# Performance work log

Hardware: AMD Instinct MI355X
Metric: run time of the kernel (lower is better)

## Reference

```python
import jax, jax.numpy as jnp
import numpy as np
import math

B = 16          # graphs per batch
N = 2048        # nodes per graph
F_IN = 64       # input node features
E_PER = 32768   # edges per graph
E = B * E_PER
H = 128         # hidden width (fixed by module)
C = 10          # output classes
K = math.ceil(0.8 * N)  # TopKPooling keep count per graph = 1639


def setup_inputs() -> dict:
    key = jax.random.key(0)
    ks = jax.random.split(key, 24)
    x = jax.random.normal(ks[0], (B * N, F_IN), jnp.float32)
    # intra-graph random edges (source->target), global node ids
    gid = jnp.repeat(jnp.arange(B, dtype=jnp.int32), E_PER)
    src = gid * N + jax.random.randint(ks[1], (E,), 0, N, dtype=jnp.int32)
    dst = gid * N + jax.random.randint(ks[2], (E,), 0, N, dtype=jnp.int32)

    def lin_w(k, o, i):
        return jax.random.normal(k, (o, i), jnp.float32) / jnp.sqrt(i)

    inp = dict(x=x, src=src, dst=dst)
    # GraphConv: lin_rel (with bias) on aggregated neighbors + lin_root (no bias)
    inp.update(W1_rel=lin_w(ks[3], H, F_IN), b1=jnp.zeros((H,), jnp.float32), W1_root=lin_w(ks[4], H, F_IN))
    inp.update(W2_rel=lin_w(ks[5], H, H), b2=jnp.zeros((H,), jnp.float32), W2_root=lin_w(ks[6], H, H))
    inp.update(W3_rel=lin_w(ks[7], H, H), b3=jnp.zeros((H,), jnp.float32), W3_root=lin_w(ks[8], H, H))
    inp.update(pool_w=jax.random.normal(ks[9], (H,), jnp.float32) / jnp.sqrt(H))
    inp.update(Wl1=lin_w(ks[10], 128, 256), bl1=jnp.zeros((128,), jnp.float32))
    inp.update(Wl2=lin_w(ks[11], 64, 128), bl2=jnp.zeros((64,), jnp.float32))
    inp.update(Wl3=lin_w(ks[12], C, 64), bl3=jnp.zeros((C,), jnp.float32))
    return inp


def _graph_conv(x, src, dst, W_rel, b, W_root, n_nodes, emask=None):
    # out_i = W_rel @ (sum_{j->i} x_j) + b + W_root @ x_i
    msg = x[src]
    if emask is not None:
        msg = msg * emask[:, None]
    agg = jax.ops.segment_sum(msg, dst, num_segments=n_nodes)
    return agg @ W_rel.T + b + x @ W_root.T


def _global_pools(x, n_per_graph):
    xb = x.reshape(B, n_per_graph, -1)
    return jnp.concatenate([xb.max(axis=1), xb.mean(axis=1)], axis=1)  # [B, 2F]


def reference(x, src, dst, W1_rel, b1, W1_root, W2_rel, b2, W2_root,
              W3_rel, b3, W3_root, pool_w, Wl1, bl1, Wl2, bl2, Wl3, bl3):
    n0 = B * N
    h = jax.nn.relu(_graph_conv(x, src, dst, W1_rel, b1, W1_root, n0))
    x1 = _global_pools(h, N)

    h = jax.nn.relu(_graph_conv(h, src, dst, W2_rel, b2, W2_root, n0))

    # TopKPooling(ratio=0.8): score = tanh(x@w/||w||); keep top-k per graph;
    # kept features scaled by score; edges with a dropped endpoint removed.
    score = jnp.tanh((h @ pool_w) / jnp.linalg.norm(pool_w))  # [B*N]
    top_s, top_i = jax.lax.top_k(score.reshape(B, N), K)      # [B,K]
    perm = (top_i + jnp.arange(B)[:, None] * N).reshape(-1)   # global old ids [B*K]
    h = h[perm] * top_s.reshape(-1)[:, None]                  # [B*K, H]

    n1 = B * K
    new_id = jnp.full((n0,), -1, jnp.int32).at[perm].set(jnp.arange(n1, dtype=jnp.int32))
    ns, nd = new_id[src], new_id[dst]
    keep = ((ns >= 0) & (nd >= 0)).astype(h.dtype)
    ns = jnp.where(ns >= 0, ns, 0)
    nd = jnp.where(nd >= 0, nd, 0)

    x2 = _global_pools(h, K)
    h = jax.nn.relu(_graph_conv(h, ns, nd, W3_rel, b3, W3_root, n1, emask=keep))
    x3 = _global_pools(h, K)

    z = x1 + x2 + x3
    z = jax.nn.relu(z @ Wl1.T + bl1)
    z = jax.nn.relu(z @ Wl2.T + bl2)
    return jax.nn.log_softmax(z @ Wl3.T + bl3, axis=-1)  # [B, C]
```

## Files before the change

kernel.cpp:

```cpp
#include <hip/hip_runtime.h>
#include <hip/hip_bf16.h>
#include <math.h>

#define NB 32768
#define NN 2048
#define BG 16
#define KK 1639
#define KKP 1664
#define N1 (BG*KK)
#define N1P (BG*KKP)
#define EE 524288
#define HH 128
#define FIN 64

using half8 = __attribute__((ext_vector_type(8))) _Float16;
using half4 = __attribute__((ext_vector_type(4))) _Float16;
using f32x4 = __attribute__((ext_vector_type(4))) float;

__device__ __forceinline__ void acc4(f32x4& a, const float4& v) {
  a[0] += v.x; a[1] += v.y; a[2] += v.z; a[3] += v.w;
}

__global__ void deg_kernel(const int* __restrict__ dst, int* deg, int n) {
  int e = blockIdx.x * blockDim.x + threadIdx.x;
  if (e < n) atomicAdd(&deg[dst[e]], 1);
}

__global__ void exscan_kernel(const int* __restrict__ deg, int* rs, int* cursor, int n) {
  __shared__ int wsum[16];
  __shared__ int carry;
  int t = threadIdx.x;
  int lane = t & 63, wid = t >> 6;
  if (t == 0) carry = 0;
  __syncthreads();
  int ntiles = (n + 4095) >> 12;
  for (int tile = 0; tile < ntiles; ++tile) {
    int idx = (tile << 12) + t * 4;
    int4 v4 = *(const int4*)(deg + idx);
    int v0 = (idx + 0 < n) ? v4.x : 0;
    int v1 = (idx + 1 < n) ? v4.y : 0;
    int v2 = (idx + 2 < n) ? v4.z : 0;
    int v3 = (idx + 3 < n) ? v4.w : 0;
    int s = v0 + v1 + v2 + v3;
    int pre = s;
#pragma unroll
    for (int off = 1; off < 64; off <<= 1) {
      int u = __shfl_up(pre, off, 64);
      if (lane >= off) pre += u;
    }
    if (lane == 63) wsum[wid] = pre;
    __syncthreads();
    int wbase = 0;
#pragma unroll
    for (int ww = 0; ww < 16; ++ww)
      if (ww < wid) wbase += wsum[ww];
    int ex = carry + wbase + (pre - s);
    int4 e4 = make_int4(ex, ex + v0, ex + v0 + v1, ex + v0 + v1 + v2);
    if (idx + 3 < n) {
      *(int4*)(rs + idx) = e4;
      *(int4*)(cursor + idx) = e4;
    } else {
      if (idx + 0 < n) { rs[idx + 0] = e4.x; cursor[idx + 0] = e4.x; }
      if (idx + 1 < n) { rs[idx + 1] = e4.y; cursor[idx + 1] = e4.y; }
      if (idx + 2 < n) { rs[idx + 2] = e4.z; cursor[idx + 2] = e4.z; }
    }
    int tot = 0;
    if (t == 1023) tot = ex + s;
    __syncthreads();
    if (t == 1023) carry = tot;
    __syncthreads();
  }
  if (t == 0) rs[n] = carry;
}

__global__ void scatter_kernel(const int* __restrict__ src, const int* __restrict__ dst,
                               int* cursor, int* csr, int n) {
  int e = blockIdx.x * blockDim.x + threadIdx.x;
  if (e < n) {
    int d = dst[e];
    int p = atomicAdd(&cursor[d], 1);
    csr[p] = src[e];
  }
}

__global__ void remap_kernel(const int* __restrict__ csr1, const int* __restrict__ new_id,
                             int* __restrict__ csr3, int n) {
  int e = blockIdx.x * blockDim.x + threadIdx.x;
  if (e < n) csr3[e] = new_id[csr1[e]];
}

template <int KD1, int KD2, int POOL, int SCORE, int REMAP>
__global__ __launch_bounds__(512, 4) void conv_mfma(
    const float* __restrict__ feat, const float* __restrict__ xr,
    const int* __restrict__ rs, const int* __restrict__ csr,
    const int* __restrict__ rows3, const int* __restrict__ rowe3,
    const _Float16* __restrict__ Wh, const _Float16* __restrict__ Wl,
    const float* __restrict__ bias, float* __restrict__ out, int M, int nwg,
    float* __restrict__ pmax, float* __restrict__ psum,
    const float* __restrict__ pw, float* __restrict__ score) {
  constexpr int KTOT = KD1 + KD2;
  constexpr int NSTEP = KTOT / 32;
  __shared__ _Float16 ah_lds[64 * KTOT];
  __shared__ _Float16 al_lds[64 * KTOT];
  __shared__ float sdot[64][8];
  __shared__ float swsq[8];

  int tid = threadIdx.x;
  int lane = tid & 63, wid = tid >> 6;
  int bq = nwg >> 3, br = nwg & 7, bx = blockIdx.x & 7, bi = blockIdx.x >> 3;
  int swz = (bx < br ? bx * (bq + 1) : br * (bq + 1) + (bx - br) * bq) + bi;
  int row0 = swz * 64;
  int ch0 = wid * 16;
  int col = lane & 15;
  int kseg = (lane >> 4) * 8;

  {
    constexpr int CH = KD1 / 4;
    constexpr int EPW = 64 / CH;
    int sub = lane / CH;
    int ch = lane % CH;
    const float4* feat4 = (const float4*)feat;
#pragma unroll
    for (int rr = 0; rr < 8; ++rr) {
      int gr = wid * 8 + rr;
      int grow = row0 + gr;
      int e0, e1;
      if (REMAP) {
        e0 = rows3[grow];
        e1 = rowe3[grow];
      } else {
        if (grow >= M) grow = M - 1;
        e0 = rs[grow];
        e1 = rs[grow + 1];
      }
      f32x4 a0 = {0.f, 0.f, 0.f, 0.f}, a1 = a0, a2 = a0, a3 = a0;
      int e = e0 + sub;
      for (; e + 7 * EPW < e1; e += 8 * EPW) {
        int c[8];
#pragma unroll
        for (int u = 0; u < 8; ++u) c[u] = csr[e + u * EPW];
        float4 v[8];
#pragma unroll
        for (int u = 0; u < 8; ++u) {
          int ci = (REMAP && c[u] < 0) ? 0 : c[u];
          v[u] = feat4[(size_t)ci * CH + ch];
        }
        if (REMAP) {
#pragma unroll
          for (int u = 0; u < 8; ++u)
            if (c[u] < 0) v[u] = make_float4(0.f, 0.f, 0.f, 0.f);
        }
        acc4(a0, v[0]); acc4(a1, v[1]); acc4(a2, v[2]); acc4(a3, v[3]);
        acc4(a0, v[4]); acc4(a1, v[5]); acc4(a2, v[6]); acc4(a3, v[7]);
      }
      for (; e + 3 * EPW < e1; e += 4 * EPW) {
        int c[4];
#pragma unroll
        for (int u = 0; u < 4; ++u) c[u] = csr[e + u * EPW];
        float4 v[4];
#pragma unroll
        for (int u = 0; u < 4; ++u) {
          int ci = (REMAP && c[u] < 0) ? 0 : c[u];
          v[u] = feat4[(size_t)ci * CH + ch];
        }
        if (REMAP) {
#pragma unroll
          for (int u = 0; u < 4; ++u)
            if (c[u] < 0) v[u] = make_float4(0.f, 0.f, 0.f, 0.f);
        }
        acc4(a0, v[0]); acc4(a1, v[1]); acc4(a2, v[2]); acc4(a3, v[3]);
      }
      for (; e < e1; e += EPW) {
        int c = csr[e];
        if (REMAP && c < 0) continue;
        float4 v = feat4[(size_t)c * CH + ch];
        acc4(a0, v);
      }
      f32x4 s = (a0 + a1) + (a2 + a3);
      if (EPW == 4) {
#pragma unroll
        for (int j = 0; j < 4; ++j) s[j] += __shfl_xor(s[j], 16, 64);
      }
#pragma unroll
      for (int j = 0; j < 4; ++j) s[j] += __shfl_xor(s[j], 32, 64);
      if (sub == 0) {
        half4 hi, lo;
#pragma unroll
        for (int j = 0; j < 4; ++j) {
          _Float16 h = (_Float16)s[j];
          hi[j] = h;
          lo[j] = (_Float16)(s[j] - (float)h);
        }
        int byte = ((gr * KTOT + ch * 4) * 2) ^ ((gr & 7) << 4);
        *(half4*)((char*)ah_lds + byte) = hi;
        *(half4*)((char*)al_lds + byte) = lo;
      }
    }
  }

  for (int idx = tid; idx < 64 * KD2 / 8; idx += 512) {
    int row = idx / (KD2 / 8);
    int kc = (idx % (KD2 / 8)) * 8;
    int grow = row0 + row;
    if (grow >= M) grow = M - 1;
    const float* sp = xr + (size_t)grow * KD2 + kc;
    float4 a0 = *(const float4*)sp;
    float4 a1 = *(const float4*)(sp + 4);
    float av[8] = {a0.x, a0.y, a0.z, a0.w, a1.x, a1.y, a1.z, a1.w};
    half8 vh, vl;
#pragma unroll
    for (int j = 0; j < 8; ++j) {
      _Float16 h = (_Float16)av[j];
      vh[j] = h;
      vl[j] = (_Float16)(av[j] - (float)h);
    }
    int byte = ((row * KTOT + KD1 + kc) * 2) ^ ((row & 7) << 4);
    *(half8*)((char*)ah_lds + byte) = vh;
    *(half8*)((char*)al_lds + byte) = vl;
  }

  size_t wbase = (size_t)(ch0 + col) * KTOT + kseg;
  half8 whc = *(const half8*)(Wh + wbase);
  half8 wlc = *(const half8*)(Wl + wbase);
  __syncthreads();

  f32x4 acc[4];
#pragma unroll
  for (int rf = 0; rf < 4; ++rf) acc[rf] = (f32x4){0.f, 0.f, 0.f, 0.f};
  int r = lane & 15;
#pragma unroll
  for (int s = 0; s < NSTEP; ++s) {
    half8 whn, wln;
    if (s + 1 < NSTEP) {
      whn = *(const half8*)(Wh + wbase + (s + 1) * 32);
      wln = *(const half8*)(Wl + wbase + (s + 1) * 32);
    }
#pragma unroll
    for (int rf = 0; rf < 4; ++rf) {
      int row = rf * 16 + r;
      int byte = ((row * KTOT + s * 32 + kseg) * 2) ^ ((row & 7) << 4);
      half8 a_h = *(const half8*)((const char*)ah_lds + byte);
      half8 a_l = *(const half8*)((const char*)al_lds + byte);
      acc[rf] = __builtin_amdgcn_mfma_f32_16x16x32_f16(a_l, whc, acc[rf], 0, 0, 0);
      acc[rf] = __builtin_amdgcn_mfma_f32_16x16x32_f16(a_h, wlc, acc[rf], 0, 0, 0);
      acc[rf] = __builtin_amdgcn_mfma_f32_16x16x32_f16(a_h, whc, acc[rf], 0, 0, 0);
    }
    if (s + 1 < NSTEP) { whc = whn; wlc = wln; }
  }

  float bv = bias[ch0 + col];
  float cmax = -3.402823466e38f, csum = 0.f;
  float wcol = SCORE ? pw[ch0 + col] : 0.f;
  float pd[4][4];
  int g = 0, rowbase = 0;
  if (POOL == 2) { g = row0 / KKP; rowbase = row0 - g * KKP; }
#pragma unroll
  for (int rf = 0; rf < 4; ++rf) {
    int orow0 = row0 + rf * 16 + (lane >> 4) * 4;
#pragma unroll
    for (int rr = 0; rr < 4; ++rr) {
      int orow = orow0 + rr;
      float v = fmaxf(acc[rf][rr] + bv, 0.f);
      if (orow < M) out[(size_t)orow * HH + ch0 + col] = v;
      if (POOL == 1) { cmax = fmaxf(cmax, v); csum += v; }
      if (POOL == 2) {
        int local = rowbase + rf * 16 + (lane >> 4) * 4 + rr;
        if (local < KK) { cmax = fmaxf(cmax, v); csum += v; }
      }
      if (SCORE) pd[rf][rr] = v * wcol;
    }
  }
  if (POOL) {
    cmax = fmaxf(cmax, __shfl_xor(cmax, 16, 64)); csum += __shfl_xor(csum, 16, 64);
    cmax = fmaxf(cmax, __shfl_xor(cmax, 32, 64)); csum += __shfl_xor(csum, 32, 64);
    if ((lane >> 4) == 0) {
      if (POOL == 1) {
        int gg = row0 >> 11, sb = (row0 & 2047) >> 6;
        pmax[(gg * 32 + sb) * HH + ch0 + col] = cmax;
        psum[(gg * 32 + sb) * HH + ch0 + col] = csum;
      } else {
        int sb = rowbase >> 6;
        pmax[(g * 26 + sb) * HH + ch0 + col] = cmax;
        psum[(g * 26 + sb) * HH + ch0 + col] = csum;
      }
    }
  }
  if (SCORE) {
#pragma unroll
    for (int rf = 0; rf < 4; ++rf)
#pragma unroll
      for (int rr = 0; rr < 4; ++rr) {
        float d = pd[rf][rr];
        d += __shfl_xor(d, 1, 64); d += __shfl_xor(d, 2, 64);
        d += __shfl_xor(d, 4, 64); d += __shfl_xor(d, 8, 64);
        if (col == 0) sdot[rf * 16 + (lane >> 4) * 4 + rr][wid] = d;
      }
    float wsq = wcol * wcol;
    wsq += __shfl_xor(wsq, 1, 64); wsq += __shfl_xor(wsq, 2, 64);
    wsq += __shfl_xor(wsq, 4, 64); wsq += __shfl_xor(wsq, 8, 64);
    if (lane == 0) swsq[wid] = wsq;
    __syncthreads();
    if (tid < 64) {
      float d = 0.f, q = 0.f;
#pragma unroll
      for (int wv = 0; wv < 8; ++wv) { d += sdot[tid][wv]; q += swsq[wv]; }
      score[row0 + tid] = tanhf(d * rsqrtf(q));
    }
  }
}

__global__ void prep_kernel(const float* __restrict__ W1_rel, const float* __restrict__ W1_root,
                            const float* __restrict__ W2_rel, const float* __restrict__ W2_root,
                            const float* __restrict__ W3_rel, const float* __restrict__ W3_root,
                            _Float16* wh1, _Float16* wl1, _Float16* wh2, _Float16* wl2,
                            _Float16* wh3, _Float16* wl3,
                            int* __restrict__ deg1, int* __restrict__ new_id,
                            int* __restrict__ rows3, int* __restrict__ rowe3) {
  int idx = blockIdx.x * blockDim.x + threadIdx.x;
  if (idx < NB + 4096) deg1[idx] = 0;
  if (idx < NB) new_id[idx] = -1;
  if (idx < N1P) { rows3[idx] = 0; rowe3[idx] = 0; }
  float v;
  _Float16* ph;
  _Float16* pl;
  int j;
  if (idx < 128 * 128) {
    j = idx;
    int o = j >> 7, k = j & 127;
    v = (k < 64) ? W1_rel[o * 64 + k] : W1_root[o * 64 + (k - 64)];
    ph = wh1; pl = wl1;
  } else if (idx < 128 * 128 + 128 * 256) {
    j = idx - 128 * 128;
    int o = j >> 8, k = j & 255;
    v = (k < 128) ? W2_rel[o * 128 + k] : W2_root[o * 128 + (k - 128)];
    ph = wh2; pl = wl2;
  } else if (idx < 128 * 128 + 2 * 128 * 256) {
    j = idx - 128 * 128 - 128 * 256;
    int o = j >> 8, k = j & 255;
    v = (k < 128) ? W3_rel[o * 128 + k] : W3_root[o * 128 + (k - 128)];
    ph = wh3; pl = wl3;
  } else {
    return;
  }
  _Float16 h = (_Float16)v;
  ph[j] = h;
  pl[j] = (_Float16)(v - (float)h);
}

__global__ void topk_kernel(const float* __restrict__ score, int* perm) {
  __shared__ unsigned long long keys[NN];
  __shared__ int hist[256];
  __shared__ unsigned long long sP;
  __shared__ int srem;
  __shared__ int scnt;
  int b = blockIdx.x, t = threadIdx.x;
  for (int i = t; i < NN; i += 256) {
    float s = score[b * NN + i];
    unsigned u = __float_as_uint(s);
    u = (u & 0x80000000u) ? ~u : (u | 0x80000000u);
    keys[i] = ((unsigned long long)u << 32) | (unsigned)(NN - 1 - i);
  }
  if (t == 0) { sP = 0ULL; srem = KK; scnt = 0; }
  __syncthreads();
  for (int pass = 0; pass < 8; ++pass) {
    int shift = 56 - 8 * pass;
    for (int i = t; i < 256; i += 256) hist[i] = 0;
    __syncthreads();
    unsigned long long P = sP;
    unsigned long long hm = (pass == 0) ? 0ULL : (~0ULL) << (shift + 8);
    for (int i = t; i < NN; i += 256) {
      unsigned long long k = keys[i];
      if (((k ^ P) & hm) == 0) atomicAdd(&hist[(int)((k >> shift) & 255)], 1);
    }
    __syncthreads();
    if (t < 64) {
      int l = t;
      int c[4], part = 0;
#pragma unroll
      for (int q = 0; q < 4; ++q) { c[q] = hist[255 - (l * 4 + q)]; part += c[q]; }
      int pre = part;
#pragma unroll
      for (int off = 1; off < 64; off <<= 1) {
        int u2 = __shfl_up(pre, off, 64);
        if (l >= off) pre += u2;
      }
      int excl = pre - part;
      int rem = srem;
      if (excl < rem && rem <= excl + part) {
        int run = excl;
#pragma unroll
        for (int q = 0; q < 4; ++q) {
          if (run + c[q] >= rem) {
            srem = rem - run;
            sP = sP | ((unsigned long long)(255 - (l * 4 + q)) << shift);
            break;
          }
          run += c[q];
        }
      }
    }
    __syncthreads();
  }
  unsigned long long T = sP;
  for (int i = t; i < NN; i += 256) {
    if (keys[i] >= T) {
      int pos = atomicAdd(&scnt, 1);
      perm[b * KK + pos] = b * NN + (NN - 1 - (int)(keys[i] & 0xffffffffULL));
    }
  }
}

__global__ void h3_kernel(const float4* __restrict__ h2, const int* __restrict__ perm,
                          const float* __restrict__ score, const int* __restrict__ rs1,
                          float4* __restrict__ h3, int* __restrict__ new_id,
                          int* __restrict__ rows3, int* __restrict__ rowe3) {
  int idx = blockIdx.x * blockDim.x + threadIdx.x;
  if (idx < N1 * 32) {
    int g = idx >> 5, c = idx & 31;
    int b = g / KK, j = g - b * KK;
    int p = perm[g];
    int pj = b * KKP + j;
    if (c == 0) {
      new_id[p] = pj;
      rows3[pj] = rs1[p];
      rowe3[pj] = rs1[p + 1];
    }
    float s = score[p];
    float4 v = h2[(size_t)p * 32 + c];
    v.x *= s; v.y *= s; v.z *= s; v.w *= s;
    h3[(size_t)pj * 32 + c] = v;
  }
}

__global__ void pool2_kernel(const float* __restrict__ h, float* pmax, float* psum) {
  int b = blockIdx.x / 26, s = blockIdx.x % 26;
  int f = threadIdx.x;
  int r0 = s * 64, r1 = min(KK, r0 + 64);
  float m = -3.402823466e38f, sum = 0.f;
  for (int r = r0; r < r1; ++r) {
    float v = h[(size_t)(b * KKP + r) * HH + f];
    m = fmaxf(m, v);
    sum += v;
  }
  pmax[(b * 26 + s) * HH + f] = m;
  psum[(b * 26 + s) * HH + f] = sum;
}

__global__ void mlp_kernel(const float* __restrict__ pm1, const float* __restrict__ ps1,
                           const float* __restrict__ pm2, const float* __restrict__ ps2,
                           const float* __restrict__ pm3, const float* __restrict__ ps3,
                           const float* __restrict__ Wl1, const float* __restrict__ bl1,
                           const float* __restrict__ Wl2, const float* __restrict__ bl2,
                           const float* __restrict__ Wl3, const float* __restrict__ bl3,
                           float* out) {
  __shared__ float z[256], a1[128], a2[64], a3[10], red[2];
  int b = blockIdx.x, t = threadIdx.x;
  float m1 = -3.402823466e38f, m2 = m1, m3 = m1;
  float s1 = 0.f, s2 = 0.f, s3 = 0.f;
  for (int s = 0; s < 32; ++s) {
    int o = (b * 32 + s) * 128 + t;
    m1 = fmaxf(m1, pm1[o]); s1 += ps1[o];
  }
  for (int s = 0; s < 26; ++s) {
    int o = (b * 26 + s) * 128 + t;
    m2 = fmaxf(m2, pm2[o]); s2 += ps2[o];
    m3 = fmaxf(m3, pm3[o]); s3 += ps3[o];
  }
  z[t] = m1 + m2 + m3;
  z[128 + t] = s1 * (1.f / NN) + (s2 + s3) * (1.f / KK);
  __syncthreads();
  {
    float acc = bl1[t];
    for (int q = 0; q < 256; ++q) acc = fmaf(Wl1[t * 256 + q], z[q], acc);
    a1[t] = fmaxf(acc, 0.f);
  }
  __syncthreads();
  if (t < 64) {
    float acc = bl2[t];
    for (int q = 0; q < 128; ++q) acc = fmaf(Wl2[t * 128 + q], a1[q], acc);
    a2[t] = fmaxf(acc, 0.f);
  }
  __syncthreads();
  if (t < 10) {
    float acc = bl3[t];
    for (int q = 0; q < 64; ++q) acc = fmaf(Wl3[t * 64 + q], a2[q], acc);
    a3[t] = acc;
  }
  __syncthreads();
  if (t == 0) {
    float m = a3[0];
    for (int i = 1; i < 10; ++i) m = fmaxf(m, a3[i]);
    float s = 0.f;
    for (int i = 0; i < 10; ++i) s += expf(a3[i] - m);
    red[0] = m;
    red[1] = logf(s);
  }
  __syncthreads();
  if (t < 10) out[b * 10 + t] = a3[t] - red[0] - red[1];
}

extern "C" void kernel_launch(void* const* d_in, const int* in_sizes, int n_in,
                              void* d_out, int out_size, void* d_ws, size_t ws_size,
                              hipStream_t stream) {
  const float* x       = (const float*)d_in[0];
  const int*   src     = (const int*)d_in[1];
  const int*   dst     = (const int*)d_in[2];
  const float* W1_rel  = (const float*)d_in[3];
  const float* b1      = (const float*)d_in[4];
  const float* W1_root = (const float*)d_in[5];
  const float* W2_rel  = (const float*)d_in[6];
  const float* b2      = (const float*)d_in[7];
  const float* W2_root = (const float*)d_in[8];
  const float* W3_rel  = (const float*)d_in[9];
  const float* b3      = (const float*)d_in[10];
  const float* W3_root = (const float*)d_in[11];
  const float* pool_w  = (const float*)d_in[12];
  const float* Wl1     = (const float*)d_in[13];
  const float* bl1     = (const float*)d_in[14];
  const float* Wl2     = (const float*)d_in[15];
  const float* bl2     = (const float*)d_in[16];
  const float* Wl3     = (const float*)d_in[17];
  const float* bl3     = (const float*)d_in[18];
  float* out = (float*)d_out;

  char* w = (char*)d_ws;
  size_t off = 0;
  auto alloc = [&](size_t bytes) -> char* {
    off = (off + 255) & ~(size_t)255;
    char* p = w + off;
    off += bytes;
    return p;
  };
  int* deg1     = (int*)alloc((NB + 4096) * 4);
  int* rs1      = (int*)alloc((NB + 1) * 4);
  int* cursor1  = (int*)alloc(NB * 4);
  int* csr1     = (int*)alloc((size_t)EE * 4);
  int* csr3     = (int*)alloc((size_t)EE * 4);
  int* new_id   = (int*)alloc(NB * 4);
  int* perm     = (int*)alloc(N1 * 4);
  int* rows3    = (int*)alloc(N1P * 4);
  int* rowe3    = (int*)alloc(N1P * 4);
  _Float16* wh1 = (_Float16*)alloc(128 * 128 * 2);
  _Float16* wl1 = (_Float16*)alloc(128 * 128 * 2);
  _Float16* wh2 = (_Float16*)alloc(128 * 256 * 2);
  _Float16* wl2 = (_Float16*)alloc(128 * 256 * 2);
  _Float16* wh3 = (_Float16*)alloc(128 * 256 * 2);
  _Float16* wl3 = (_Float16*)alloc(128 * 256 * 2);
  float* bufA   = (float*)alloc((size_t)NB * HH * 4);
  float* bufB   = (float*)alloc((size_t)NB * HH * 4);
  float* score  = (float*)alloc(NB * 4);
  float* pm1    = (float*)alloc(BG * 32 * HH * 4);
  float* ps1    = (float*)alloc(BG * 32 * HH * 4);
  float* pm2    = (float*)alloc(BG * 26 * HH * 4);
  float* ps2    = (float*)alloc(BG * 26 * HH * 4);
  float* pm3    = (float*)alloc(BG * 26 * HH * 4);
  float* ps3    = (float*)alloc(BG * 26 * HH * 4);
  if (off > ws_size) return;

  const int TB = 256;
  const int egrid = (EE + TB - 1) / TB;

  prep_kernel<<<(128 * 128 + 2 * 128 * 256 + TB - 1) / TB, TB, 0, stream>>>(
      W1_rel, W1_root, W2_rel, W2_root, W3_rel, W3_root, wh1, wl1, wh2, wl2, wh3, wl3,
      deg1, new_id, rows3, rowe3);

  deg_kernel<<<egrid, TB, 0, stream>>>(dst, deg1, EE);
  exscan_kernel<<<1, 1024, 0, stream>>>(deg1, rs1, cursor1, NB);
  scatter_kernel<<<egrid, TB, 0, stream>>>(src, dst, cursor1, csr1, EE);

  conv_mfma<64, 64, 1, 0, 0><<<NB / 64, 512, 0, stream>>>(
      x, x, rs1, csr1, nullptr, nullptr, wh1, wl1, b1, bufA, NB, NB / 64, pm1, ps1,
      nullptr, nullptr);

  conv_mfma<128, 128, 0, 1, 0><<<NB / 64, 512, 0, stream>>>(
      bufA, bufA, rs1, csr1, nullptr, nullptr, wh2, wl2, b2, bufB, NB, NB / 64,
      nullptr, nullptr, pool_w, score);

  topk_kernel<<<BG, 256, 0, stream>>>(score, perm);
  h3_kernel<<<(N1 * 32 + TB - 1) / TB, TB, 0, stream>>>((const float4*)bufB, perm, score,
                                                        rs1, (float4*)bufA, new_id,
                                                        rows3, rowe3);
  remap_kernel<<<egrid, TB, 0, stream>>>(csr1, new_id, csr3, EE);
  pool2_kernel<<<BG * 26, 128, 0, stream>>>(bufA, pm2, ps2);

  conv_mfma<128, 128, 2, 0, 2><<<N1P / 64, 512, 0, stream>>>(
      bufA, bufA, nullptr, csr3, rows3, rowe3, wh3, wl3, b3, bufB, N1P, N1P / 64, pm3, ps3,
      nullptr, nullptr);

  mlp_kernel<<<BG, 128, 0, stream>>>(pm1, ps1, pm2, ps2, pm3, ps3,
                                     Wl1, bl1, Wl2, bl2, Wl3, bl3, out);
}
```

Baseline: 220.5 us.

## Gather neighbor features from fp16 copies in graph conv aggregation

Adds fp16 shadow copies of the input features, the layer-1 output and the pooled layer-3 input. The conv kernels now gather neighbor rows from these half-precision buffers, eight halves per lane, and accumulate in fp32. This halves the bytes moved by the edge gather, which is the dominant memory cost. The price is extra fp16 writes in the producer kernels and a larger prep grid. Rounding the gathered features to fp16 loses precision compared with the former hi/lo fp32 path.

```diff
diff --git a/kernel.cpp b/kernel.cpp
--- a/kernel.cpp
+++ b/kernel.cpp
@@ -16,10 +16,6 @@
 using half8 = __attribute__((ext_vector_type(8))) _Float16;
 using half4 = __attribute__((ext_vector_type(4))) _Float16;
 using f32x4 = __attribute__((ext_vector_type(4))) float;
-
-__device__ __forceinline__ void acc4(f32x4& a, const float4& v) {
-  a[0] += v.x; a[1] += v.y; a[2] += v.z; a[3] += v.w;
-}
 
 __global__ void deg_kernel(const int* __restrict__ dst, int* deg, int n) {
   int e = blockIdx.x * blockDim.x + threadIdx.x;
@@ -89,13 +85,14 @@
   if (e < n) csr3[e] = new_id[csr1[e]];
 }
 
-template <int KD1, int KD2, int POOL, int SCORE, int REMAP>
+template <int KD1, int KD2, int POOL, int SCORE, int REMAP, int OUT16>
 __global__ __launch_bounds__(512, 4) void conv_mfma(
-    const float* __restrict__ feat, const float* __restrict__ xr,
+    const _Float16* __restrict__ feat, const float* __restrict__ xr,
     const int* __restrict__ rs, const int* __restrict__ csr,
     const int* __restrict__ rows3, const int* __restrict__ rowe3,
     const _Float16* __restrict__ Wh, const _Float16* __restrict__ Wl,
-    const float* __restrict__ bias, float* __restrict__ out, int M, int nwg,
+    const float* __restrict__ bias, float* __restrict__ out,
+    _Float16* __restrict__ out16, int M, int nwg,
     float* __restrict__ pmax, float* __restrict__ psum,
     const float* __restrict__ pw, float* __restrict__ score) {
   constexpr int KTOT = KD1 + KD2;
@@ -115,11 +112,11 @@
   int kseg = (lane >> 4) * 8;
 
   {
-    constexpr int CH = KD1 / 4;
-    constexpr int EPW = 64 / CH;
-    int sub = lane / CH;
-    int ch = lane % CH;
-    const float4* feat4 = (const float4*)feat;
+    constexpr int CH16 = KD1 / 8;
+    constexpr int EPW = 64 / CH16;
+    int sub = lane / CH16;
+    int ch = lane % CH16;
+    const half8* feat16 = (const half8*)feat;
 #pragma unroll
     for (int rr = 0; rr < 8; ++rr) {
       int gr = wid * 8 + rr;
@@ -133,67 +130,82 @@
         e0 = rs[grow];
         e1 = rs[grow + 1];
       }
-      f32x4 a0 = {0.f, 0.f, 0.f, 0.f}, a1 = a0, a2 = a0, a3 = a0;
+      f32x4 sA0 = {0.f, 0.f, 0.f, 0.f}, sB0 = sA0, sA1 = sA0, sB1 = sA0;
       int e = e0 + sub;
       for (; e + 7 * EPW < e1; e += 8 * EPW) {
         int c[8];
 #pragma unroll
         for (int u = 0; u < 8; ++u) c[u] = csr[e + u * EPW];
-        float4 v[8];
+        half8 v[8];
 #pragma unroll
         for (int u = 0; u < 8; ++u) {
           int ci = (REMAP && c[u] < 0) ? 0 : c[u];
-          v[u] = feat4[(size_t)ci * CH + ch];
+          v[u] = feat16[(size_t)ci * CH16 + ch];
         }
-        if (REMAP) {
-#pragma unroll
-          for (int u = 0; u < 8; ++u)
-            if (c[u] < 0) v[u] = make_float4(0.f, 0.f, 0.f, 0.f);
+#pragma unroll
+        for (int u = 0; u < 8; ++u) {
+          if (REMAP && c[u] < 0) continue;
+          if (u & 1) {
+#pragma unroll
+            for (int j = 0; j < 4; ++j) { sA1[j] += (float)v[u][j]; sB1[j] += (float)v[u][4 + j]; }
+          } else {
+#pragma unroll
+            for (int j = 0; j < 4; ++j) { sA0[j] += (float)v[u][j]; sB0[j] += (float)v[u][4 + j]; }
+          }
         }
-        acc4(a0, v[0]); acc4(a1, v[1]); acc4(a2, v[2]); acc4(a3, v[3]);
-        acc4(a0, v[4]); acc4(a1, v[5]); acc4(a2, v[6]); acc4(a3, v[7]);
       }
       for (; e + 3 * EPW < e1; e += 4 * EPW) {
         int c[4];
 #pragma unroll
         for (int u = 0; u < 4; ++u) c[u] = csr[e + u * EPW];
-        float4 v[4];
+        half8 v[4];
 #pragma unroll
         for (int u = 0; u < 4; ++u) {
           int ci = (REMAP && c[u] < 0) ? 0 : c[u];
-          v[u] = feat4[(size_t)ci * CH + ch];
+          v[u] = feat16[(size_t)ci * CH16 + ch];
         }
-        if (REMAP) {
-#pragma unroll
-          for (int u = 0; u < 4; ++u)
-            if (c[u] < 0) v[u] = make_float4(0.f, 0.f, 0.f, 0.f);
+#pragma unroll
+        for (int u = 0; u < 4; ++u) {
+          if (REMAP && c[u] < 0) continue;
+          if (u & 1) {
+#pragma unroll
+            for (int j = 0; j < 4; ++j) { sA1[j] += (float)v[u][j]; sB1[j] += (float)v[u][4 + j]; }
+          } else {
+#pragma unroll
+            for (int j = 0; j < 4; ++j) { sA0[j] += (float)v[u][j]; sB0[j] += (float)v[u][4 + j]; }
+          }
         }
-        acc4(a0, v[0]); acc4(a1, v[1]); acc4(a2, v[2]); acc4(a3, v[3]);
       }
       for (; e < e1; e += EPW) {
         int c = csr[e];
         if (REMAP && c < 0) continue;
-        float4 v = feat4[(size_t)c * CH + ch];
-        acc4(a0, v);
-      }
-      f32x4 s = (a0 + a1) + (a2 + a3);
-      if (EPW == 4) {
-#pragma unroll
-        for (int j = 0; j < 4; ++j) s[j] += __shfl_xor(s[j], 16, 64);
-      }
-#pragma unroll
-      for (int j = 0; j < 4; ++j) s[j] += __shfl_xor(s[j], 32, 64);
+        half8 v = feat16[(size_t)c * CH16 + ch];
+#pragma unroll
+        for (int j = 0; j < 4; ++j) { sA0[j] += (float)v[j]; sB0[j] += (float)v[4 + j]; }
+      }
+      f32x4 sA = sA0 + sA1, sB = sB0 + sB1;
+#pragma unroll
+      for (int off = CH16; off < 64; off <<= 1) {
+#pragma unroll
+        for (int j = 0; j < 4; ++j) {
+          sA[j] += __shfl_xor(sA[j], off, 64);
+          sB[j] += __shfl_xor(sB[j], off, 64);
+        }
+      }
       if (sub == 0) {
-        half4 hi, lo;
+        half8 hi, lo;
 #pragma unroll
         for (int j = 0; j < 4; ++j) {
-          _Float16 h = (_Float16)s[j];
-          hi[j] = h;
-          lo[j] = (_Float16)(s[j] - (float)h);
+          _Float16 hA = (_Float16)sA[j];
+          hi[j] = hA;
+          lo[j] = (_Float16)(sA[j] - (float)hA);
+          _Float16 hB = (_Float16)sB[j];
+          hi[4 + j] = hB;
+          lo[4 + j] = (_Float16)(sB[j] - (float)hB);
         }
-        int byte = ((gr * KTOT + ch * 4) * 2) ^ ((gr & 7) << 4);
-        *(half4*)((char*)ah_lds + byte) = hi;
-        *(half4*)((char*)al_lds + byte) = lo;
+        int byte = ((gr * KTOT + ch * 8) * 2) ^ ((gr & 7) << 4);
+        *(half8*)((char*)ah_lds + byte) = hi;
+        *(half8*)((char*)al_lds + byte) = lo;
       }
     }
   }
@@ -261,7 +273,10 @@
     for (int rr = 0; rr < 4; ++rr) {
       int orow = orow0 + rr;
       float v = fmaxf(acc[rf][rr] + bv, 0.f);
-      if (orow < M) out[(size_t)orow * HH + ch0 + col] = v;
+      if (orow < M) {
+        out[(size_t)orow * HH + ch0 + col] = v;
+        if (OUT16) out16[(size_t)orow * HH + ch0 + col] = (_Float16)v;
+      }
       if (POOL == 1) { cmax = fmaxf(cmax, v); csum += v; }
       if (POOL == 2) {
         int local = rowbase + rf * 16 + (lane >> 4) * 4 + rr;
@@ -312,11 +327,20 @@
 __global__ void prep_kernel(const float* __restrict__ W1_rel, const float* __restrict__ W1_root,
                             const float* __restrict__ W2_rel, const float* __restrict__ W2_root,
                             const float* __restrict__ W3_rel, const float* __restrict__ W3_root,
+                            const float* __restrict__ x,
                             _Float16* wh1, _Float16* wl1, _Float16* wh2, _Float16* wl2,
-                            _Float16* wh3, _Float16* wl3,
+                            _Float16* wh3, _Float16* wl3, _Float16* __restrict__ xh,
                             int* __restrict__ deg1, int* __restrict__ new_id,
                             int* __restrict__ rows3, int* __restrict__ rowe3) {
   int idx = blockIdx.x * blockDim.x + threadIdx.x;
+  if (idx < NB * FIN / 8) {
+    float4 a0 = *(const float4*)(x + idx * 8);
+    float4 a1 = *(const float4*)(x + idx * 8 + 4);
+    half8 h;
+    h[0] = (_Float16)a0.x; h[1] = (_Float16)a0.y; h[2] = (_Float16)a0.z; h[3] = (_Float16)a0.w;
+    h[4] = (_Float16)a1.x; h[5] = (_Float16)a1.y; h[6] = (_Float16)a1.z; h[7] = (_Float16)a1.w;
+    *(half8*)(xh + idx * 8) = h;
+  }
   if (idx < NB + 4096) deg1[idx] = 0;
   if (idx < NB) new_id[idx] = -1;
   if (idx < N1P) { rows3[idx] = 0; rowe3[idx] = 0; }
@@ -412,7 +436,8 @@
 
 __global__ void h3_kernel(const float4* __restrict__ h2, const int* __restrict__ perm,
                           const float* __restrict__ score, const int* __restrict__ rs1,
-                          float4* __restrict__ h3, int* __restrict__ new_id,
+                          float4* __restrict__ h3, _Float16* __restrict__ h3h,
+                          int* __restrict__ new_id,
                           int* __restrict__ rows3, int* __restrict__ rowe3) {
   int idx = blockIdx.x * blockDim.x + threadIdx.x;
   if (idx < N1 * 32) {
@@ -429,6 +454,10 @@
     float4 v = h2[(size_t)p * 32 + c];
     v.x *= s; v.y *= s; v.z *= s; v.w *= s;
     h3[(size_t)pj * 32 + c] = v;
+    half4 hv;
+    hv[0] = (_Float16)v.x; hv[1] = (_Float16)v.y;
+    hv[2] = (_Float16)v.z; hv[3] = (_Float16)v.w;
+    *(half4*)(h3h + (size_t)pj * HH + c * 4) = hv;
   }
 }
 
@@ -546,6 +575,9 @@
   _Float16* wl2 = (_Float16*)alloc(128 * 256 * 2);
   _Float16* wh3 = (_Float16*)alloc(128 * 256 * 2);
   _Float16* wl3 = (_Float16*)alloc(128 * 256 * 2);
+  _Float16* xh  = (_Float16*)alloc((size_t)NB * FIN * 2);
+  _Float16* h1h = (_Float16*)alloc((size_t)NB * HH * 2);
+  _Float16* h3h = (_Float16*)alloc((size_t)N1P * HH * 2);
   float* bufA   = (float*)alloc((size_t)NB * HH * 4);
   float* bufB   = (float*)alloc((size_t)NB * HH * 4);
   float* score  = (float*)alloc(NB * 4);
@@ -560,32 +592,32 @@
   const int TB = 256;
   const int egrid = (EE + TB - 1) / TB;
 
-  prep_kernel<<<(128 * 128 + 2 * 128 * 256 + TB - 1) / TB, TB, 0, stream>>>(
-      W1_rel, W1_root, W2_rel, W2_root, W3_rel, W3_root, wh1, wl1, wh2, wl2, wh3, wl3,
-      deg1, new_id, rows3, rowe3);
+  prep_kernel<<<(NB * FIN / 8 + TB - 1) / TB, TB, 0, stream>>>(
+      W1_rel, W1_root, W2_rel, W2_root, W3_rel, W3_root, x,
+      wh1, wl1, wh2, wl2, wh3, wl3, xh, deg1, new_id, rows3, rowe3);
 
   deg_kernel<<<egrid, TB, 0, stream>>>(dst, deg1, EE);
   exscan_kernel<<<1, 1024, 0, stream>>>(deg1, rs1, cursor1, NB);
   scatter_kernel<<<egrid, TB, 0, stream>>>(src, dst, cursor1, csr1, EE);
 
-  conv_mfma<64, 64, 1, 0, 0><<<NB / 64, 512, 0, stream>>>(
-      x, x, rs1, csr1, nullptr, nullptr, wh1, wl1, b1, bufA, NB, NB / 64, pm1, ps1,
+  conv_mfma<64, 64, 1, 0, 0, 1><<<NB / 64, 512, 0, stream>>>(
+      xh, x, rs1, csr1, nullptr, nullptr, wh1, wl1, b1, bufA, h1h, NB, NB / 64, pm1, ps1,
       nullptr, nullptr);
 
-  conv_mfma<128, 128, 0, 1, 0><<<NB / 64, 512, 0, stream>>>(
-      bufA, bufA, rs1, csr1, nullptr, nullptr, wh2, wl2, b2, bufB, NB, NB / 64,
+  conv_mfma<128, 128, 0, 1, 0, 0><<<NB / 64, 512, 0, stream>>>(
+      h1h, bufA, rs1, csr1, nullptr, nullptr, wh2, wl2, b2, bufB, nullptr, NB, NB / 64,
       nullptr, nullptr, pool_w, score);
 
   topk_kernel<<<BG, 256, 0, stream>>>(score, perm);
   h3_kernel<<<(N1 * 32 + TB - 1) / TB, TB, 0, stream>>>((const float4*)bufB, perm, score,
-                                                        rs1, (float4*)bufA, new_id,
+                                                        rs1, (float4*)bufA, h3h, new_id,
                                                         rows3, rowe3);
   remap_kernel<<<egrid, TB, 0, stream>>>(csr1, new_id, csr3, EE);
   pool2_kernel<<<BG * 26, 128, 0, stream>>>(bufA, pm2, ps2);
 
-  conv_mfma<128, 128, 2, 0, 2><<<N1P / 64, 512, 0, stream>>>(
-      bufA, bufA, nullptr, csr3, rows3, rowe3, wh3, wl3, b3, bufB, N1P, N1P / 64, pm3, ps3,
-      nullptr, nullptr);
+  conv_mfma<128, 128, 2, 0, 2, 0><<<N1P / 64, 512, 0, stream>>>(
+      h3h, bufA, nullptr, csr3, rows3, rowe3, wh3, wl3, b3, bufB, nullptr, N1P, N1P / 64,
+      pm3, ps3, nullptr, nullptr);
 
   mlp_kernel<<<BG, 128, 0, stream>>>(pm1, ps1, pm2, ps2, pm3, ps3,
                                      Wl1, bl1, Wl2, bl2, Wl3, bl3, out);
```

Result: no change. 220.8 us (+0.1%).
